# Kernel tuning notes

Hardware: AMD Instinct MI355X
Metric: run time of the kernel (lower is better)

Reference implementation:

```python
import jax, jax.numpy as jnp
from jax import lax
import numpy as np

K_SIZE = 3  # deformable kernel size
PAD = 1
STRIDE = 1


def _conv3x3(x, w, b):
    # plain 3x3 conv, pad 1, stride 1, NCHW/OIHW
    y = lax.conv_general_dilated(x, w, window_strides=(1, 1),
                                 padding=[(1, 1), (1, 1)],
                                 dimension_numbers=('NCHW', 'OIHW', 'NCHW'))
    return y + b[None, :, None, None]


def _deform_sample(x, py, px):
    """Bilinear sample x [B,C,H,W] at float coords py,px [B,K,Ho,Wo].
    Out-of-bounds samples contribute zero (matches torchvision deform_conv2d).
    Returns [B,C,K,Ho,Wo]."""
    B, C, H, W = x.shape
    y0 = jnp.floor(py)
    x0 = jnp.floor(px)
    gat = jax.vmap(lambda img, iy, ix: img[:, iy, ix])  # per-batch gather -> [C,K,Ho,Wo]
    out = jnp.zeros((B, C) + py.shape[1:], dtype=x.dtype)
    for yc, xc in ((y0, x0), (y0, x0 + 1), (y0 + 1, x0), (y0 + 1, x0 + 1)):
        wgt = (1.0 - jnp.abs(py - yc)) * (1.0 - jnp.abs(px - xc))
        valid = (yc >= 0) & (yc <= H - 1) & (xc >= 0) & (xc <= W - 1)
        wgt = jnp.where(valid, wgt, 0.0)
        iy = jnp.clip(yc, 0, H - 1).astype(jnp.int32)
        ix = jnp.clip(xc, 0, W - 1).astype(jnp.int32)
        out = out + wgt[:, None] * gat(x, iy, ix)
    return out


def reference(x, w_off, b_off, w_mask, b_mask, w_dcn, b_dcn):
    k = K_SIZE
    K = k * k
    B, C, H, W = x.shape
    # offset conv (2*K channels: (dy, dx) pairs per kernel position, row-major)
    offset = _conv3x3(x, w_off, b_off)            # [B, 2K, H, W]
    mask = jax.nn.sigmoid(_conv3x3(x, w_mask, b_mask))  # [B, K, H, W]
    off = offset.reshape(B, K, 2, H, W)
    dy, dx = off[:, :, 0], off[:, :, 1]
    ki = (jnp.arange(K) // k).astype(x.dtype)  # kernel row index
    kj = (jnp.arange(K) % k).astype(x.dtype)   # kernel col index
    # sampling coordinates: out position * stride - pad + kernel pos + learned offset
    py = (jnp.arange(H, dtype=x.dtype)[None, None, :, None] * STRIDE - PAD
          + ki[None, :, None, None] + dy)
    px = (jnp.arange(W, dtype=x.dtype)[None, None, None, :] * STRIDE - PAD
          + kj[None, :, None, None] + dx)
    val = _deform_sample(x, py, px) * mask[:, None]   # [B,C,K,H,W]
    Cout = w_dcn.shape[0]
    out = jnp.einsum('ock,bckhw->bohw', w_dcn.reshape(Cout, C, K), val)
    return out + b_dcn[None, :, None, None]


def setup_inputs() -> dict:
    key = jax.random.key(0)
    ks = jax.random.split(key, 6)
    B, C, Cout, H, W, k = 4, 256, 256, 64, 64, 3
    K = k * k
    x = jax.random.normal(ks[0], (B, C, H, W), dtype=jnp.float32)
    # NOTE: original inits offset/mask conv to zeros (degenerate -> plain conv).
    # Use small random weights so offsets/masks are nontrivial but local.
    w_off = jax.random.normal(ks[1], (2 * K, C, 3, 3), dtype=jnp.float32) * 0.01
    b_off = jnp.zeros((2 * K,), dtype=jnp.float32)
    w_mask = jax.random.normal(ks[2], (K, C, 3, 3), dtype=jnp.float32) * 0.01
    b_mask = jnp.zeros((K,), dtype=jnp.float32)
    fan_in = C * K
    w_dcn = jax.random.normal(ks[3], (Cout, C, 3, 3), dtype=jnp.float32) / np.sqrt(fan_in)
    b_dcn = jnp.zeros((Cout,), dtype=jnp.float32)
    return {"x": x, "w_off": w_off, "b_off": b_off, "w_mask": w_mask,
            "b_mask": b_mask, "w_dcn": w_dcn, "b_dcn": b_dcn}
```

## Files before the change

kernel.cpp:

```cpp
#include <hip/hip_runtime.h>
#include <math.h>

#define B_ 4
#define C_ 256
#define CO_ 256
#define H_ 64
#define W_ 64
#define HW_ 4096
#define KK_ 9
#define NCH_ 27

typedef __attribute__((ext_vector_type(8))) short bf16x8;
typedef __attribute__((ext_vector_type(4))) float f32x4;

__device__ inline unsigned short f32_to_bf16(float f) {
    unsigned int u = __float_as_uint(f);
    unsigned int r = (u + 0x7FFFu + ((u >> 16) & 1u)) >> 16;
    return (unsigned short)r;
}

__global__ void prep_all(const float* __restrict__ x, unsigned short* __restrict__ xTh,
                         const float* __restrict__ w_dcn, const float* __restrict__ w_off,
                         const float* __restrict__ w_mask,
                         unsigned short* __restrict__ wTs, unsigned short* __restrict__ wCs) {
    __shared__ float tile[32][33];
    __shared__ float lw[2304];
    const int t = threadIdx.x;
    const int bid = blockIdx.x;
    if (bid < 4096) {
        const int tx = t & 31, ty = t >> 5;
        const int b = bid >> 10;
        const int rem = bid & 1023;
        const int c0 = (rem >> 7) << 5;
        const int hw0 = (rem & 127) << 5;
        const float* xb = x + ((size_t)b << 20);
        unsigned short* xTb = xTh + ((size_t)b << 20);
#pragma unroll
        for (int r = 0; r < 4; ++r) {
            int row = ty + (r << 3);
            tile[row][tx] = xb[((size_t)(c0 + row) << 12) + hw0 + tx];
        }
        __syncthreads();
#pragma unroll
        for (int r = 0; r < 4; ++r) {
            int row = ty + (r << 3);
            xTb[((size_t)(hw0 + row) << 8) + c0 + tx] = f32_to_bf16(tile[tx][row]);
        }
    } else if (bid < 4352) {
        const int o = bid - 4096;
        for (int e = t; e < 2304; e += 256) lw[e] = w_dcn[(size_t)o * 2304 + e];
        __syncthreads();
        for (int e = t; e < 2304; e += 256) {
            int k = e >> 8, c = e & 255;
            int chunk = (k << 2) + (c >> 6), ck = c & 63;
            int pos = (o << 6) + (((ck >> 3) ^ (o & 7)) << 3) + (ck & 7);
            wTs[(size_t)chunk * 16384 + pos] = f32_to_bf16(lw[c * 9 + k]);
        }
    } else {
        const int ch = bid - 4352;
        const float* src = (ch < 18) ? w_off + (size_t)ch * 2304
                         : (ch < NCH_) ? w_mask + (size_t)(ch - 18) * 2304
                         : nullptr;
        for (int e = t; e < 2304; e += 256) lw[e] = src ? src[e] : 0.f;
        __syncthreads();
        for (int e = t; e < 2304; e += 256) {
            int k = e >> 8, c = e & 255;
            int chunk = (k << 2) + (c >> 6), ck = c & 63;
            int pos = (ch << 6) + (((ck >> 3) ^ (ch & 7)) << 3) + (ck & 7);
            wCs[(size_t)chunk * 2048 + pos] = f32_to_bf16(lw[c * 9 + k]);
        }
    }
}

__global__ __launch_bounds__(256, 2) void conv_mfma(
    const unsigned short* __restrict__ xTh, const unsigned short* __restrict__ wCs,
    const float* __restrict__ b_off, const float* __restrict__ b_mask,
    float* __restrict__ offmask) {
    __shared__ alignas(16) unsigned short wlds[2][2048];
    __shared__ alignas(16) unsigned short xlds[2][2048];
    const int t = threadIdx.x;
    const int bid = blockIdx.x;
    const int b = (bid & 7) >> 1;
    const int ph = bid & 1;
    const int hh = bid >> 3;
    const unsigned short* xb = xTh + ((size_t)b << 20);

    auto stage_w = [&](int chunk, int buf) {
        const unsigned short* g = wCs + ((size_t)chunk << 11) + (t << 3);
        __builtin_amdgcn_global_load_lds(
            (const __attribute__((address_space(1))) unsigned int*)g,
            (__attribute__((address_space(3))) unsigned int*)&wlds[buf][t << 3], 16, 0, 0);
    };

    auto stage_x = [&](int chunk, int buf) {
        int k = chunk >> 2, cc = chunk & 3;
        int ki = k / 3, kj = k % 3;
        int py = hh + ki - 1;
        int p = t >> 3, cs = t & 7;
        int px = (ph << 5) + p + kj - 1;
        uint4 u = make_uint4(0u, 0u, 0u, 0u);
        if (py >= 0 && py < H_ && px >= 0 && px < W_)
            u = *(const uint4*)(xb + (((size_t)((py << 6) + px)) << 8) + (cc << 6) + (cs << 3));
        *(uint4*)&xlds[buf][(p << 6) + ((cs ^ (p & 7)) << 3)] = u;
    };

    const int wid = t >> 6, lane = t & 63;
    const int wc = wid >> 1, wp = wid & 1;
    const int m16 = lane & 15, kg = lane >> 4;
    f32x4 acc = {};

    stage_w(0, 0);
    stage_x(0, 0);
    __syncthreads();

    for (int chunk = 0; chunk < 36; ++chunk) {
        int cur = chunk & 1, nxt = cur ^ 1;
        if (chunk < 35) { stage_w(chunk + 1, nxt); stage_x(chunk + 1, nxt); }
#pragma unroll
        for (int ks = 0; ks < 2; ++ks) {
            int s = (ks << 2) + kg;
            int o = (wc << 4) + m16;
            bf16x8 a = *(const bf16x8*)&wlds[cur][(o << 6) + ((s ^ (o & 7)) << 3)];
            int p = (wp << 4) + m16;
            bf16x8 bf = *(const bf16x8*)&xlds[cur][(p << 6) + ((s ^ (p & 7)) << 3)];
            acc = __builtin_amdgcn_mfma_f32_16x16x32_bf16(a, bf, acc, 0, 0, 0);
        }
        __syncthreads();
    }

    const int pix = (hh << 6) + (ph << 5) + (wp << 4) + m16;
#pragma unroll
    for (int r = 0; r < 4; ++r) {
        int ch = (wc << 4) + (kg << 2) + r;
        if (ch < NCH_) {
            float bias = (ch < 18) ? b_off[ch] : b_mask[ch - 18];
            offmask[(((size_t)b * NCH_ + ch) << 12) + pix] = acc[r] + bias;
        }
    }
}

__global__ __launch_bounds__(512, 1) void dcn_fused(
    const unsigned short* __restrict__ xTh, const float* __restrict__ offmask,
    const unsigned short* __restrict__ wTs, const float* __restrict__ b_dcn,
    float* __restrict__ out) {
    __shared__ float4 cw[576];
    __shared__ ushort4 coff[576];
    __shared__ alignas(16) unsigned short wbuf[3][16384];
    __shared__ alignas(16) unsigned short vbuf[4096];

    const int t = threadIdx.x;
    const int bid = blockIdx.x;
    const int b = (bid & 7) >> 1;
    const int tile64 = (bid >> 3) + ((bid & 1) << 5);
    const int pix0 = tile64 << 6;
    const unsigned short* xb = xTh + ((size_t)b << 20);
    const float* omb = offmask + (((size_t)b * NCH_) << 12);

    for (int e = t; e < 576; e += 512) {
        int k = e >> 6, p = e & 63;
        int pix = pix0 + p;
        int hh = pix >> 6, ww = pix & 63;
        float dy = omb[((size_t)(2 * k) << 12) + pix];
        float dx = omb[((size_t)(2 * k + 1) << 12) + pix];
        float ml = omb[((size_t)(18 + k) << 12) + pix];
        float m = 1.f / (1.f + __expf(-ml));
        float py = (float)(hh - 1 + (k / 3)) + dy;
        float px = (float)(ww - 1 + (k % 3)) + dx;
        float fy0 = floorf(py), fx0 = floorf(px);
        float ay = py - fy0, ax = px - fx0;
        bool y0v = (fy0 >= 0.f) && (fy0 <= 63.f);
        bool y1v = (fy0 >= -1.f) && (fy0 <= 62.f);
        bool x0v = (fx0 >= 0.f) && (fx0 <= 63.f);
        bool x1v = (fx0 >= -1.f) && (fx0 <= 62.f);
        int y0 = (int)fy0, x0 = (int)fx0;
        int iy0 = min(max(y0, 0), 63), iy1 = min(max(y0 + 1, 0), 63);
        int ix0 = min(max(x0, 0), 63), ix1 = min(max(x0 + 1, 0), 63);
        float w00 = (y0v && x0v) ? m * (1.f - ay) * (1.f - ax) : 0.f;
        float w01 = (y0v && x1v) ? m * (1.f - ay) * ax : 0.f;
        float w10 = (y1v && x0v) ? m * ay * (1.f - ax) : 0.f;
        float w11 = (y1v && x1v) ? m * ay * ax : 0.f;
        cw[e] = make_float4(w00, w01, w10, w11);
        coff[e] = make_ushort4((unsigned short)((iy0 << 6) + ix0),
                               (unsigned short)((iy0 << 6) + ix1),
                               (unsigned short)((iy1 << 6) + ix0),
                               (unsigned short)((iy1 << 6) + ix1));
    }

    const int oct = t & 7, pq = t >> 3;
    const int wid = t >> 6, lane = t & 63;
    const int wo = wid >> 1, wp = wid & 1;
    const int m16 = lane & 15, kg = lane >> 4;

    auto stage_w = [&](int chunk, int slot) {
#pragma unroll
        for (int r = 0; r < 4; ++r) {
            int off16 = (r << 9) + t;
            const unsigned short* g = wTs + ((size_t)chunk << 14) + (off16 << 3);
            __builtin_amdgcn_global_load_lds(
                (const __attribute__((address_space(1))) unsigned int*)g,
                (__attribute__((address_space(3))) unsigned int*)&wbuf[slot][off16 << 3], 16, 0, 0);
        }
    };

    auto gather = [&](int chunk, uint4* g) {
        int k = chunk >> 2, cc = chunk & 3;
        ushort4 o4 = coff[(k << 6) + pq];
        const unsigned short* cb = xb + (cc << 6) + (oct << 3);
        g[0] = *(const uint4*)(cb + ((int)o4.x << 8));
        g[1] = *(const uint4*)(cb + ((int)o4.y << 8));
        g[2] = *(const uint4*)(cb + ((int)o4.z << 8));
        g[3] = *(const uint4*)(cb + ((int)o4.w << 8));
    };

    auto finish = [&](int chunk, const uint4* g) {
        int k = chunk >> 2;
        float4 w4 = cw[(k << 6) + pq];
        union { uint4 v; unsigned int u[4]; } A, B2, C2, D2;
        A.v = g[0]; B2.v = g[1]; C2.v = g[2]; D2.v = g[3];
        unsigned short o8[8];
#pragma unroll
        for (int j = 0; j < 4; ++j) {
            float al = __uint_as_float(A.u[j] << 16);
            float ah = __uint_as_float(A.u[j] & 0xffff0000u);
            float bl = __uint_as_float(B2.u[j] << 16);
            float bh = __uint_as_float(B2.u[j] & 0xffff0000u);
            float cl = __uint_as_float(C2.u[j] << 16);
            float ch = __uint_as_float(C2.u[j] & 0xffff0000u);
            float dl = __uint_as_float(D2.u[j] << 16);
            float dh = __uint_as_float(D2.u[j] & 0xffff0000u);
            float vl = w4.x * al + w4.y * bl + w4.z * cl + w4.w * dl;
            float vh = w4.x * ah + w4.y * bh + w4.z * ch + w4.w * dh;
            o8[2 * j]     = f32_to_bf16(vl);
            o8[2 * j + 1] = f32_to_bf16(vh);
        }
        *(uint4*)&vbuf[(pq << 6) + ((oct ^ (pq & 7)) << 3)] = *(const uint4*)o8;
    };

    f32x4 acc[4][2] = {};

    auto compute = [&](int slot) {
#pragma unroll
        for (int ks = 0; ks < 2; ++ks) {
            int s = (ks << 2) + kg;
            bf16x8 aF[4], bF[2];
#pragma unroll
            for (int i = 0; i < 4; ++i) {
                int o = (wo << 6) + (i << 4) + m16;
                aF[i] = *(const bf16x8*)&wbuf[slot][(o << 6) + ((s ^ (o & 7)) << 3)];
            }
#pragma unroll
            for (int j = 0; j < 2; ++j) {
                int p = (wp << 5) + (j << 4) + m16;
                bF[j] = *(const bf16x8*)&vbuf[(p << 6) + ((s ^ (p & 7)) << 3)];
            }
#pragma unroll
            for (int i = 0; i < 4; ++i)
#pragma unroll
                for (int j = 0; j < 2; ++j)
                    acc[i][j] = __builtin_amdgcn_mfma_f32_16x16x32_bf16(
                        aF[i], bF[j], acc[i][j], 0, 0, 0);
        }
    };

    uint4 gA[4], gB[4];

    __syncthreads();
    gather(0, gA);
    stage_w(0, 0);
    stage_w(1, 1);

#define HALF(CUR, GCUR, GNXT, NW)                                        \
    __builtin_amdgcn_s_barrier();                                        \
    asm volatile("" ::: "memory");                                       \
    if ((CUR) + 1 < 36) gather((CUR) + 1, GNXT);                         \
    if ((CUR) + 2 < 36) stage_w((CUR) + 2, ((CUR) + 2) % 3);             \
    asm volatile("s_waitcnt vmcnt(" #NW ")" ::: "memory");               \
    finish((CUR), GCUR);                                                 \
    asm volatile("s_waitcnt lgkmcnt(0)" ::: "memory");                   \
    __builtin_amdgcn_s_barrier();                                        \
    asm volatile("" ::: "memory");                                       \
    compute((CUR) % 3);

    for (int c = 0; c < 34; c += 2) {
        HALF(c, gA, gB, 12)
        HALF(c + 1, gB, gA, 12)
    }
    HALF(34, gA, gB, 8)
    HALF(35, gB, gA, 0)
#undef HALF

#pragma unroll
    for (int i = 0; i < 4; ++i) {
        int ob = (wo << 6) + (i << 4) + (kg << 2);
#pragma unroll
        for (int j = 0; j < 2; ++j) {
            int p = pix0 + (wp << 5) + (j << 4) + m16;
#pragma unroll
            for (int r = 0; r < 4; ++r) {
                int oo = ob + r;
                out[(((size_t)(b << 8) + oo) << 12) + p] = acc[i][j][r] + b_dcn[oo];
            }
        }
    }
}

extern "C" void kernel_launch(void* const* d_in, const int* in_sizes, int n_in,
                              void* d_out, int out_size, void* d_ws, size_t ws_size,
                              hipStream_t stream) {
    const float* x      = (const float*)d_in[0];
    const float* w_off  = (const float*)d_in[1];
    const float* b_off  = (const float*)d_in[2];
    const float* w_mask = (const float*)d_in[3];
    const float* b_mask = (const float*)d_in[4];
    const float* w_dcn  = (const float*)d_in[5];
    const float* b_dcn  = (const float*)d_in[6];
    float* out = (float*)d_out;

    float* ws = (float*)d_ws;
    float* offmask = ws;
    unsigned short* xTh = (unsigned short*)(offmask + (size_t)B_ * NCH_ * HW_);
    unsigned short* wTs = xTh + ((size_t)B_ * HW_ * C_);
    unsigned short* wCs = wTs + (size_t)36 * 16384;

    prep_all<<<dim3(4384), dim3(256), 0, stream>>>(x, xTh, w_dcn, w_off, w_mask, wTs, wCs);
    conv_mfma<<<dim3(512), dim3(256), 0, stream>>>(xTh, wCs, b_off, b_mask, offmask);
    dcn_fused<<<dim3(256), dim3(512), 0, stream>>>(xTh, offmask, wTs, b_dcn, out);
}
```

Measured before the change: 78.89 us.

## Split DCN reduction over channel halves with partial buffers and combine kernel

The deformable-conv GEMM kernel is split along the input-channel dimension into two halves, doubling the grid to 512 blocks. Each block writes fp32 partial sums, and a new combine kernel adds the two halves plus the bias. The kernel also stores bilinear weights as bf16 and sample coordinates as bytes, drops from triple to double weight buffering to cut LDS use, raises the launch-bounds occupancy hint, and packs the output with v_cvt_pk_bf16_f32. The aim is better CU occupancy and latency hiding, at the cost of 32MB of partial-sum traffic, an extra launch, and slightly less precise bilinear weights.

```diff
diff --git a/kernel.cpp b/kernel.cpp
--- a/kernel.cpp
+++ b/kernel.cpp
@@ -139,19 +139,19 @@
     }
 }
 
-__global__ __launch_bounds__(512, 1) void dcn_fused(
+__global__ __launch_bounds__(512, 4) void dcn_fused(
     const unsigned short* __restrict__ xTh, const float* __restrict__ offmask,
-    const unsigned short* __restrict__ wTs, const float* __restrict__ b_dcn,
-    float* __restrict__ out) {
-    __shared__ float4 cw[576];
-    __shared__ ushort4 coff[576];
-    __shared__ alignas(16) unsigned short wbuf[3][16384];
+    const unsigned short* __restrict__ wTs, float* __restrict__ part) {
+    __shared__ ushort4 cwh[576];
+    __shared__ uchar4 coffb[576];
+    __shared__ alignas(16) unsigned short wbuf[2][16384];
     __shared__ alignas(16) unsigned short vbuf[4096];
 
     const int t = threadIdx.x;
     const int bid = blockIdx.x;
     const int b = (bid & 7) >> 1;
-    const int tile64 = (bid >> 3) + ((bid & 1) << 5);
+    const int half = bid & 1;
+    const int tile64 = bid >> 3;
     const int pix0 = tile64 << 6;
     const unsigned short* xb = xTh + ((size_t)b << 20);
     const float* omb = offmask + (((size_t)b * NCH_) << 12);
@@ -179,45 +179,50 @@
         float w01 = (y0v && x1v) ? m * (1.f - ay) * ax : 0.f;
         float w10 = (y1v && x0v) ? m * ay * (1.f - ax) : 0.f;
         float w11 = (y1v && x1v) ? m * ay * ax : 0.f;
-        cw[e] = make_float4(w00, w01, w10, w11);
-        coff[e] = make_ushort4((unsigned short)((iy0 << 6) + ix0),
-                               (unsigned short)((iy0 << 6) + ix1),
-                               (unsigned short)((iy1 << 6) + ix0),
-                               (unsigned short)((iy1 << 6) + ix1));
+        cwh[e] = make_ushort4(f32_to_bf16(w00), f32_to_bf16(w01),
+                              f32_to_bf16(w10), f32_to_bf16(w11));
+        coffb[e] = make_uchar4((unsigned char)iy0, (unsigned char)ix0,
+                               (unsigned char)iy1, (unsigned char)ix1);
     }
 
     const int oct = t & 7, pq = t >> 3;
     const int wid = t >> 6, lane = t & 63;
     const int wo = wid >> 1, wp = wid & 1;
     const int m16 = lane & 15, kg = lane >> 4;
-
-    auto stage_w = [&](int chunk, int slot) {
+    const int vslot = (pq << 6) + ((oct ^ (pq & 7)) << 3);
+
+    auto stage_w = [&](int c, int slot) {
+        int gc = ((c >> 1) << 2) + (half << 1) + (c & 1);
 #pragma unroll
         for (int r = 0; r < 4; ++r) {
             int off16 = (r << 9) + t;
-            const unsigned short* g = wTs + ((size_t)chunk << 14) + (off16 << 3);
+            const unsigned short* g = wTs + ((size_t)gc << 14) + (off16 << 3);
             __builtin_amdgcn_global_load_lds(
                 (const __attribute__((address_space(1))) unsigned int*)g,
                 (__attribute__((address_space(3))) unsigned int*)&wbuf[slot][off16 << 3], 16, 0, 0);
         }
     };
 
-    auto gather = [&](int chunk, uint4* g) {
-        int k = chunk >> 2, cc = chunk & 3;
-        ushort4 o4 = coff[(k << 6) + pq];
+    auto gather = [&](int c, uint4* g) {
+        int k = c >> 1, cc = (half << 1) + (c & 1);
+        uchar4 q = coffb[(k << 6) + pq];
         const unsigned short* cb = xb + (cc << 6) + (oct << 3);
-        g[0] = *(const uint4*)(cb + ((int)o4.x << 8));
-        g[1] = *(const uint4*)(cb + ((int)o4.y << 8));
-        g[2] = *(const uint4*)(cb + ((int)o4.z << 8));
-        g[3] = *(const uint4*)(cb + ((int)o4.w << 8));
-    };
-
-    auto finish = [&](int chunk, const uint4* g) {
-        int k = chunk >> 2;
-        float4 w4 = cw[(k << 6) + pq];
+        g[0] = *(const uint4*)(cb + ((((int)q.x << 6) + q.y) << 8));
+        g[1] = *(const uint4*)(cb + ((((int)q.x << 6) + q.w) << 8));
+        g[2] = *(const uint4*)(cb + ((((int)q.z << 6) + q.y) << 8));
+        g[3] = *(const uint4*)(cb + ((((int)q.z << 6) + q.w) << 8));
+    };
+
+    auto finish = [&](int c, const uint4* g) {
+        int k = c >> 1;
+        ushort4 wv = cwh[(k << 6) + pq];
+        float w0 = __uint_as_float((unsigned int)wv.x << 16);
+        float w1 = __uint_as_float((unsigned int)wv.y << 16);
+        float w2 = __uint_as_float((unsigned int)wv.z << 16);
+        float w3 = __uint_as_float((unsigned int)wv.w << 16);
         union { uint4 v; unsigned int u[4]; } A, B2, C2, D2;
         A.v = g[0]; B2.v = g[1]; C2.v = g[2]; D2.v = g[3];
-        unsigned short o8[8];
+        unsigned int o4[4];
 #pragma unroll
         for (int j = 0; j < 4; ++j) {
             float al = __uint_as_float(A.u[j] << 16);
@@ -228,12 +233,13 @@
             float ch = __uint_as_float(C2.u[j] & 0xffff0000u);
             float dl = __uint_as_float(D2.u[j] << 16);
             float dh = __uint_as_float(D2.u[j] & 0xffff0000u);
-            float vl = w4.x * al + w4.y * bl + w4.z * cl + w4.w * dl;
-            float vh = w4.x * ah + w4.y * bh + w4.z * ch + w4.w * dh;
-            o8[2 * j]     = f32_to_bf16(vl);
-            o8[2 * j + 1] = f32_to_bf16(vh);
-        }
-        *(uint4*)&vbuf[(pq << 6) + ((oct ^ (pq & 7)) << 3)] = *(const uint4*)o8;
+            float vl = w0 * al + w1 * bl + w2 * cl + w3 * dl;
+            float vh = w0 * ah + w1 * bh + w2 * ch + w3 * dh;
+            unsigned int pk;
+            asm("v_cvt_pk_bf16_f32 %0, %1, %2" : "=v"(pk) : "v"(vl), "v"(vh));
+            o4[j] = pk;
+        }
+        *(uint4*)&vbuf[vslot] = make_uint4(o4[0], o4[1], o4[2], o4[3]);
     };
 
     f32x4 acc[4][2] = {};
@@ -267,28 +273,27 @@
     __syncthreads();
     gather(0, gA);
     stage_w(0, 0);
-    stage_w(1, 1);
-
-#define HALF(CUR, GCUR, GNXT, NW)                                        \
+
+#define HALFSTEP(CUR, GCUR, GNXT, NW)                                    \
     __builtin_amdgcn_s_barrier();                                        \
     asm volatile("" ::: "memory");                                       \
-    if ((CUR) + 1 < 36) gather((CUR) + 1, GNXT);                         \
-    if ((CUR) + 2 < 36) stage_w((CUR) + 2, ((CUR) + 2) % 3);             \
+    if ((CUR) + 1 < 18) { gather((CUR) + 1, GNXT); stage_w((CUR) + 1, ((CUR) + 1) & 1); } \
     asm volatile("s_waitcnt vmcnt(" #NW ")" ::: "memory");               \
     finish((CUR), GCUR);                                                 \
     asm volatile("s_waitcnt lgkmcnt(0)" ::: "memory");                   \
     __builtin_amdgcn_s_barrier();                                        \
     asm volatile("" ::: "memory");                                       \
-    compute((CUR) % 3);
-
-    for (int c = 0; c < 34; c += 2) {
-        HALF(c, gA, gB, 12)
-        HALF(c + 1, gB, gA, 12)
-    }
-    HALF(34, gA, gB, 8)
-    HALF(35, gB, gA, 0)
-#undef HALF
-
+    compute((CUR) & 1);
+
+    for (int c = 0; c < 16; c += 2) {
+        HALFSTEP(c, gA, gB, 8)
+        HALFSTEP(c + 1, gB, gA, 8)
+    }
+    HALFSTEP(16, gA, gB, 8)
+    HALFSTEP(17, gB, gA, 0)
+#undef HALFSTEP
+
+    float* pd = part + (((size_t)((half << 2) + b)) << 20);
 #pragma unroll
     for (int i = 0; i < 4; ++i) {
         int ob = (wo << 6) + (i << 4) + (kg << 2);
@@ -298,10 +303,28 @@
 #pragma unroll
             for (int r = 0; r < 4; ++r) {
                 int oo = ob + r;
-                out[(((size_t)(b << 8) + oo) << 12) + p] = acc[i][j][r] + b_dcn[oo];
+                pd[(((size_t)oo) << 12) + p] = acc[i][j][r];
             }
         }
     }
+}
+
+__global__ __launch_bounds__(256) void combine_out(
+    const float* __restrict__ part, const float* __restrict__ b_dcn,
+    float* __restrict__ out) {
+    int i = (blockIdx.x * 256 + threadIdx.x) << 3;
+    float bias = b_dcn[(i >> 12) & 255];
+    const float* p1 = part + ((size_t)4 << 20);
+    float4 a0 = *(const float4*)(part + i);
+    float4 a1 = *(const float4*)(part + i + 4);
+    float4 c0 = *(const float4*)(p1 + i);
+    float4 c1 = *(const float4*)(p1 + i + 4);
+    float4 r0 = make_float4(a0.x + c0.x + bias, a0.y + c0.y + bias,
+                            a0.z + c0.z + bias, a0.w + c0.w + bias);
+    float4 r1 = make_float4(a1.x + c1.x + bias, a1.y + c1.y + bias,
+                            a1.z + c1.z + bias, a1.w + c1.w + bias);
+    *(float4*)(out + i) = r0;
+    *(float4*)(out + i + 4) = r1;
 }
 
 extern "C" void kernel_launch(void* const* d_in, const int* in_sizes, int n_in,
@@ -321,8 +344,10 @@
     unsigned short* xTh = (unsigned short*)(offmask + (size_t)B_ * NCH_ * HW_);
     unsigned short* wTs = xTh + ((size_t)B_ * HW_ * C_);
     unsigned short* wCs = wTs + (size_t)36 * 16384;
+    float* part = (float*)(wCs + (size_t)36 * 2048);
 
     prep_all<<<dim3(4384), dim3(256), 0, stream>>>(x, xTh, w_dcn, w_off, w_mask, wTs, wCs);
     conv_mfma<<<dim3(512), dim3(256), 0, stream>>>(xTh, wCs, b_off, b_mask, offmask);
-    dcn_fused<<<dim3(256), dim3(512), 0, stream>>>(xTh, offmask, wTs, b_dcn, out);
-}
+    dcn_fused<<<dim3(512), dim3(512), 0, stream>>>(xTh, offmask, wTs, part);
+    combine_out<<<dim3(2048), dim3(256), 0, stream>>>(part, b_dcn, out);
+}
```

Result: faster. 73.62 us (-6.7%).
